# Performance work log

Hardware: AMD Instinct MI355X
Metric: run time of the kernel (lower is better)

Reference implementation:

```python
import jax, jax.numpy as jnp
import numpy as np

W_WORKERS = 2
Q_LEN = 16
HIDDEN = 4096
N_HEADS = 32
N_KV = 8
HEAD_DIM = 128
L_SHARED = 8192
L_WORKER = 2048
THETA = 10000.0


def rotate_half(x):
    x1, x2 = jnp.split(x, 2, axis=-1)
    return jnp.concatenate((-x2, x1), axis=-1)


def rope_cos_sin(pos):
    # pos: int array [...]; returns cos,sin of shape [..., HEAD_DIM] (HF convention: freqs duplicated)
    inv = 1.0 / (THETA ** (jnp.arange(0, HEAD_DIM, 2, dtype=jnp.float32) / HEAD_DIM))
    ang = pos[..., None].astype(jnp.float32) * inv
    emb = jnp.concatenate((ang, ang), axis=-1)
    return jnp.cos(emb), jnp.sin(emb)


def setup_inputs() -> dict:
    key = jax.random.key(0)
    ks = jax.random.split(key, 16)
    std = 0.02
    # new keys are appended at positions L_WORKER..L_WORKER+Q-1 of each worker's own segment
    pos_new = jnp.broadcast_to(L_WORKER + jnp.arange(Q_LEN), (W_WORKERS, Q_LEN))
    cos_new, sin_new = rope_cos_sin(pos_new)
    return {
        'hidden_states': jax.random.normal(ks[0], (W_WORKERS, Q_LEN, HIDDEN), jnp.float32),
        'Wq': jax.random.normal(ks[1], (N_HEADS * HEAD_DIM, HIDDEN), jnp.float32) * std,
        'bq': jnp.zeros((N_HEADS * HEAD_DIM,), jnp.float32),
        'Wk': jax.random.normal(ks[2], (N_KV * HEAD_DIM, HIDDEN), jnp.float32) * std,
        'bk': jnp.zeros((N_KV * HEAD_DIM,), jnp.float32),
        'Wv': jax.random.normal(ks[3], (N_KV * HEAD_DIM, HIDDEN), jnp.float32) * std,
        'bv': jnp.zeros((N_KV * HEAD_DIM,), jnp.float32),
        'Wo': jax.random.normal(ks[4], (HIDDEN, N_HEADS * HEAD_DIM), jnp.float32) * std,
        'seg_shared_k': jax.random.normal(ks[5], (N_KV, L_SHARED, HEAD_DIM), jnp.float32),
        'seg_shared_v': jax.random.normal(ks[6], (N_KV, L_SHARED, HEAD_DIM), jnp.float32),
        'w0_k': jax.random.normal(ks[7], (N_KV, L_WORKER, HEAD_DIM), jnp.float32),
        'w0_v': jax.random.normal(ks[8], (N_KV, L_WORKER, HEAD_DIM), jnp.float32),
        'w1_k': jax.random.normal(ks[9], (N_KV, L_WORKER, HEAD_DIM), jnp.float32),
        'w1_v': jax.random.normal(ks[10], (N_KV, L_WORKER, HEAD_DIM), jnp.float32),
        'cos_new': cos_new,
        'sin_new': sin_new,
    }


def reference(hidden_states, Wq, bq, Wk, bk, Wv, bv, Wo,
              seg_shared_k, seg_shared_v, w0_k, w0_v, w1_k, w1_v,
              cos_new, sin_new):
    W, Q, _ = hidden_states.shape
    scale = HEAD_DIM ** -0.5
    # projections -> [W, n_heads, Q, D]
    q = (hidden_states @ Wq.T + bq).reshape(W, Q, N_HEADS, HEAD_DIM).transpose(0, 2, 1, 3)
    k_new = (hidden_states @ Wk.T + bk).reshape(W, Q, N_KV, HEAD_DIM).transpose(0, 2, 1, 3)
    v_new = (hidden_states @ Wv.T + bv).reshape(W, Q, N_KV, HEAD_DIM).transpose(0, 2, 1, 3)
    # rope new keys (unsqueeze_dim=1: broadcast over kv heads)
    c, s = cos_new[:, None], sin_new[:, None]
    k_new = k_new * c + rotate_half(k_new) * s
    # cache update: segment 0 = shared prompt, segment 1/2 = worker 0/1 own cache (grows by Q)
    keys = [seg_shared_k,
            jnp.concatenate([w0_k, k_new[0]], axis=1),
            jnp.concatenate([w1_k, k_new[1]], axis=1)]
    values = [seg_shared_v,
              jnp.concatenate([w0_v, v_new[0]], axis=1),
              jnp.concatenate([w1_v, v_new[1]], axis=1)]
    frag_lens = [L_SHARED, L_WORKER + Q, L_WORKER + Q]
    # worker w's view: [shared, other worker's cache, own cache]
    orders = [[0, 2, 1], [0, 1, 2]]
    loc = np.zeros((3, W_WORKERS, Q), dtype=np.int32)
    for w, order in enumerate(orders):
        pos = 0
        for seg in reversed(order):
            pos += frag_lens[seg]
            loc[seg, w] = np.arange(pos - Q, pos)
    loc = jnp.asarray(loc)  # [S, W, Q]
    cos_q, sin_q = rope_cos_sin(loc)  # [S, W, Q, D]
    # hogwild_rope: queries rotated per (segment, worker) location -> [S, W, H, Q, D]
    rq = q[None] * cos_q[:, :, None] + rotate_half(q)[None] * sin_q[:, :, None]
    rep = N_HEADS // N_KV
    scores, v_parts = [], []
    for seg in range(3):
        k_s = jnp.repeat(keys[seg], rep, axis=0)  # GQA expand [H, L_s, D]
        sc = jnp.einsum('whqd,hld->whql', rq[seg], k_s) * scale
        mask = jnp.arange(frag_lens[seg])[None, None, None, :] <= loc[seg][:, None, :, None]
        scores.append(jnp.where(mask, sc, jnp.finfo(sc.dtype).min))
        v_parts.append(jnp.repeat(values[seg], rep, axis=0))
    scores = jnp.concatenate(scores, axis=-1)        # [W, H, Q, Ltot] joint softmax over fragments
    probs = jax.nn.softmax(scores, axis=-1)
    v_all = jnp.concatenate(v_parts, axis=1)         # [H, Ltot, D]
    attn = jnp.einsum('whql,hld->whqd', probs, v_all)
    out = attn.transpose(0, 2, 1, 3).reshape(W, Q, N_HEADS * HEAD_DIM) @ Wo.T
    return out
```

## Files before the change

### kernel.cpp

```cpp
#include <hip/hip_runtime.h>
#include <hip/hip_fp16.h>
#include <cstdint>
#include <cstddef>

#define QL 16
#define LSH 8192
#define LWK 2048
#define SCALE 0.08838834764831845f

typedef __attribute__((ext_vector_type(8))) short short8;
typedef __attribute__((ext_vector_type(4))) short short4v;
typedef __attribute__((ext_vector_type(4))) float f32x4;
typedef __attribute__((ext_vector_type(8))) unsigned short ushort8v;

#if defined(__has_builtin)
#if __has_builtin(__builtin_amdgcn_mfma_f32_16x16x16bf16_1k)
#define HAVE_MFMA16 1
#endif
#endif

__device__ __forceinline__ unsigned short f2bf(float f) {
  unsigned int u = __float_as_uint(f);
  u += 0x7fffu + ((u >> 16) & 1u);
  return (unsigned short)(u >> 16);
}
__device__ __forceinline__ float bf2f(unsigned short b) {
  return __uint_as_float(((unsigned int)b) << 16);
}

__device__ __forceinline__ void gload_lds16(const float* g, float* lds) {
  __builtin_amdgcn_global_load_lds(
      (const __attribute__((address_space(1))) void*)g,
      (__attribute__((address_space(3))) void*)lds, 16, 0, 0);
}

__device__ __forceinline__ void gload_f4(float4& d, const float* p) {
  asm volatile("global_load_dwordx4 %0, %1, off"
               : "=v"(d)
               : "v"((const __attribute__((address_space(1))) float*)p));
}
__device__ __forceinline__ void gload_f1(float& d, const float* p) {
  asm volatile("global_load_dword %0, %1, off"
               : "=v"(d)
               : "v"((const __attribute__((address_space(1))) float*)p));
}
__device__ __forceinline__ void gload_s8(short8& d, const unsigned short* p) {
  asm volatile("global_load_dwordx4 %0, %1, off"
               : "=v"(d)
               : "v"((const __attribute__((address_space(1))) unsigned short*)p));
}

__global__ __launch_bounds__(256) void k_cast(
    const float* __restrict__ in, unsigned short* __restrict__ outp, int n4)
{
  int i = blockIdx.x * 256 + threadIdx.x;
  if (i < n4) {
    float4 v = ((const float4*)in)[i];
    ushort4 p; p.x = f2bf(v.x); p.y = f2bf(v.y); p.z = f2bf(v.z); p.w = f2bf(v.w);
    ((ushort4*)outp)[i] = p;
  }
}

__global__ __launch_bounds__(256, 2) void k_gemm4(
    const unsigned short* __restrict__ Xbf,
    const float* __restrict__ W0, const float* __restrict__ W1, const float* __restrict__ W2,
    const float* __restrict__ b0, const float* __restrict__ b1, const float* __restrict__ b2,
    float* __restrict__ outA, float* __restrict__ outB,
    float* __restrict__ outC, float* __restrict__ outD, int Ntot)
{
  __shared__ float Ws[2][16 * 516];
  const int bx = blockIdx.x;
  const int n0 = (bx >> 2) * 16;
  const int kq = bx & 3;
  const float* W; const float* bias; int row0;
  if (n0 < 4096)      { W = W0; bias = b0; row0 = n0; }
  else if (n0 < 5120) { W = W1; bias = b1; row0 = n0 - 4096; }
  else                { W = W2; bias = b2; row0 = n0 - 5120; }
  const int t = threadIdx.x;
  const int w_id = t >> 6;
  const int lane = t & 63;
  const int l15 = lane & 15;
  const int quad = lane >> 4;
  const int cb0 = kq * 1024;
  const int wk = w_id * 128;

  f32x4 C0 = {0.f,0.f,0.f,0.f}, C1 = {0.f,0.f,0.f,0.f};
  short8 xa0[2][4], xa1[2][4];

#pragma unroll
  for (int c = 0; c < 2; ++c) {
    const int cbase = cb0 + c * 512;
#pragma unroll
    for (int i = 0; i < 8; ++i) {
      int idx = w_id * 8 + i;
      int r = idx >> 1, hh = idx & 1;
      const float* g = W + (size_t)(row0 + r) * 4096 + cbase + hh * 256 + lane * 4;
      gload_lds16(g, &Ws[c][r * 516 + hh * 256]);
    }
#pragma unroll
    for (int ks = 0; ks < 4; ++ks) {
      int ko = wk + ks * 32 + quad * 8;
      gload_s8(xa0[c][ks], Xbf + (size_t)l15 * 4096 + cbase + ko);
      gload_s8(xa1[c][ks], Xbf + (size_t)(16 + l15) * 4096 + cbase + ko);
    }
  }
  __builtin_amdgcn_sched_barrier(0);
#pragma unroll
  for (int c = 0; c < 2; ++c) {
    if (c == 0) asm volatile("s_waitcnt vmcnt(16)" ::: "memory");
    else        asm volatile("s_waitcnt vmcnt(0)"  ::: "memory");
    __builtin_amdgcn_sched_barrier(0);
    __builtin_amdgcn_s_barrier();
    __builtin_amdgcn_sched_barrier(0);
    const float* Wsb = Ws[c];
#pragma unroll
    for (int ks = 0; ks < 4; ++ks) {
      int ko = wk + ks * 32 + quad * 8;
      f32x4 wlo = *(const f32x4*)(&Wsb[l15 * 516 + ko]);
      f32x4 whi = *(const f32x4*)(&Wsb[l15 * 516 + ko + 4]);
      short8 bfr;
      bfr[0] = (short)f2bf(wlo[0]); bfr[1] = (short)f2bf(wlo[1]);
      bfr[2] = (short)f2bf(wlo[2]); bfr[3] = (short)f2bf(wlo[3]);
      bfr[4] = (short)f2bf(whi[0]); bfr[5] = (short)f2bf(whi[1]);
      bfr[6] = (short)f2bf(whi[2]); bfr[7] = (short)f2bf(whi[3]);
      C0 = __builtin_amdgcn_mfma_f32_16x16x32_bf16(xa0[c][ks], bfr, C0, 0, 0, 0);
      C1 = __builtin_amdgcn_mfma_f32_16x16x32_bf16(xa1[c][ks], bfr, C1, 0, 0, 0);
    }
  }
  float* Red = &Ws[0][0];
#pragma unroll
  for (int i = 0; i < 4; ++i) {
    Red[w_id * 512 + (quad * 4 + i) * 16 + l15] = C0[i];
    Red[w_id * 512 + 256 + (quad * 4 + i) * 16 + l15] = C1[i];
  }
  __syncthreads();
  float* dst = (kq == 0) ? outA : (kq == 1) ? outB : (kq == 2) ? outC : outD;
#pragma unroll
  for (int e = t; e < 512; e += 256) {
    float s = Red[e] + Red[512 + e] + Red[1024 + e] + Red[1536 + e];
    int m = e >> 4, n = e & 15;
    if (kq == 0 && bias) s += bias[row0 + n];
    dst[(size_t)m * Ntot + n0 + n] = s;
  }
}

__global__ __launch_bounds__(256) void k_add(
    const float* __restrict__ A, const float* __restrict__ B,
    const float* __restrict__ C, const float* __restrict__ D,
    float* __restrict__ o, int n4)
{
  int i = blockIdx.x * 256 + threadIdx.x;
  if (i < n4) {
    float4 a = ((const float4*)A)[i], b = ((const float4*)B)[i];
    float4 c = ((const float4*)C)[i], d = ((const float4*)D)[i];
    float4 r;
    r.x = (a.x + b.x) + (c.x + d.x); r.y = (a.y + b.y) + (c.y + d.y);
    r.z = (a.z + b.z) + (c.z + d.z); r.w = (a.w + b.w) + (c.w + d.w);
    ((float4*)o)[i] = r;
  }
}

__global__ __launch_bounds__(256) void k_rope(
    const float* __restrict__ qA, const float* __restrict__ qB,
    const float* __restrict__ qC, const float* __restrict__ qD,
    const float* __restrict__ cosn, const float* __restrict__ sinn,
    unsigned short* __restrict__ rq, unsigned short* __restrict__ knew,
    unsigned short* __restrict__ vnew)
{
  const int g = blockIdx.x * 256 + threadIdx.x;
  const float LOGTH = 9.210340371976184f;
  if (g < 393216) {
    int d = g & 127, q = (g >> 7) & 15, head = (g >> 11) & 31, w = (g >> 16) & 1, var = g >> 17;
    int tok = w * 16 + q;
    int col = head * 128 + d;
    size_t ix = (size_t)tok * 6144 + col;
    float val = (qA[ix] + qB[ix]) + (qC[ix] + qD[ix]);
    size_t ir = (d < 64) ? ix + 64 : ix - 64;
    float rot = (qA[ir] + qB[ir]) + (qC[ir] + qD[ir]);
    if (d < 64) rot = -rot;
    int pos = (var == 0 ? 12304 : (var == 1 ? 4112 : 2048)) + q;
    int i = d & 63;
    float inv = expf(-(float)i * (LOGTH / 64.0f));
    float ang = (float)pos * inv;
    float c = cosf(ang), s = sinf(ang);
    rq[g] = f2bf((val * c + rot * s) * SCALE);
  } else {
    int g2 = g - 393216;
    if (g2 < 65536) {
      int isv = (g2 >= 32768);
      if (isv) g2 -= 32768;
      int d = g2 & 127, q = (g2 >> 7) & 15, h = (g2 >> 11) & 7, w = (g2 >> 14) & 1;
      int tok = w * 16 + q;
      if (isv) {
        size_t ix = (size_t)tok * 6144 + 5120 + h * 128 + d;
        vnew[g2] = f2bf((qA[ix] + qB[ix]) + (qC[ix] + qD[ix]));
      } else {
        size_t ix = (size_t)tok * 6144 + 4096 + h * 128 + d;
        float val = (qA[ix] + qB[ix]) + (qC[ix] + qD[ix]);
        size_t ir = (d < 64) ? ix + 64 : ix - 64;
        float rot = (qA[ir] + qB[ir]) + (qC[ir] + qD[ir]);
        if (d < 64) rot = -rot;
        float c = cosn[tok * 128 + d], s = sinn[tok * 128 + d];
        knew[g2] = f2bf(val * c + rot * s);
      }
    }
  }
}

__global__ __launch_bounds__(512, 2) void k_attn(
    const float* __restrict__ shk, const float* __restrict__ shv,
    const float* __restrict__ w0k, const float* __restrict__ w0v,
    const float* __restrict__ w1k, const float* __restrict__ w1v,
    const unsigned short* __restrict__ rq,
    const unsigned short* __restrict__ knew, const unsigned short* __restrict__ vnew,
    __half* __restrict__ accP, float* __restrict__ lP)
{
  __shared__ alignas(16) unsigned short Ks[64 * 136];
  __shared__ alignas(16) unsigned short Vts[128 * 72];
#ifndef HAVE_MFMA16
  __shared__ alignas(16) unsigned short Plds[8 * 16 * 72];
#endif

  const int h = blockIdx.x / 98;
  const int cidx = blockIdx.x % 98;
  int kind, k0, nk; bool is_new;
  if (cidx < 64)      { kind = 0; k0 = cidx * 128; nk = 128; is_new = false; }
  else if (cidx < 81) { int c = cidx - 64; kind = 1; k0 = c * 128; nk = (c == 16) ? 16 : 128; is_new = (c == 16); }
  else                { int c = cidx - 81; kind = 2; k0 = c * 128; nk = (c == 16) ? 16 : 128; is_new = (c == 16); }

  const int t = threadIdx.x;
  const int w_id = t >> 6;
  const int lane = t & 63;
  const int l15 = lane & 15;
  const int quad = lane >> 4;
  const int worker = w_id >> 2;
  const int hq = w_id & 3;
  const int col4 = t & 31;
  const int rowb = t >> 5;
  const int dv = t & 127;
  const int tg = t >> 7;

  int var; bool causal;
  if (kind == 0)      { var = 0; causal = false; }
  else if (kind == 1) { var = (worker == 0) ? 2 : 1; causal = (worker == 0); }
  else                { var = (worker == 1) ? 2 : 1; causal = (worker == 1); }

  const float* Ksrc = (kind == 0) ? (shk + (size_t)h * LSH * 128)
                     : (kind == 1) ? (w0k + (size_t)h * LWK * 128)
                                   : (w1k + (size_t)h * LWK * 128);
  const float* Vsrc = (kind == 0) ? (shv + (size_t)h * LSH * 128)
                     : (kind == 1) ? (w0v + (size_t)h * LWK * 128)
                                   : (w1v + (size_t)h * LWK * 128);
  const int wseg = (kind == 2) ? 1 : 0;
  const unsigned short* knsrc = knew + ((size_t)wseg * 8 + h) * 16 * 128;
  const unsigned short* vnsrc = vnew + ((size_t)wseg * 8 + h) * 16 * 128;

  const int head = h * 4 + hq;
  short8 arq[4];
  {
    const unsigned short* base =
        rq + ((((size_t)var * 2 + worker) * 32 + head) * 16 + l15) * 128 + quad * 8;
#pragma unroll
    for (int ks = 0; ks < 4; ++ks) arq[ks] = *(const short8*)(base + ks * 32);
  }

  float lrow = 0.f;
  f32x4 acc[8];
#pragma unroll
  for (int dt = 0; dt < 8; ++dt) acc[dt] = {0.f,0.f,0.f,0.f};

  float4 kf[4];
  float  vf[16];

  const float* kbase = Ksrc + (size_t)(k0 + rowb) * 128 + col4 * 4;
  const float* vbase = Vsrc + (size_t)(k0 + tg * 8) * 128 + dv;

  auto issue_tile = [&](int st) {
    const float* kp = kbase + (size_t)st * 64 * 128;
#pragma unroll
    for (int i = 0; i < 4; ++i) gload_f4(kf[i], kp + (size_t)i * 16 * 128);
    const float* vp = vbase + (size_t)st * 64 * 128;
#pragma unroll
    for (int g = 0; g < 2; ++g)
#pragma unroll
      for (int i = 0; i < 8; ++i)
        gload_f1(vf[g * 8 + i], vp + (size_t)(g * 32 + i) * 128);
  };

  auto lds_write = [&]() {
#pragma unroll
    for (int i = 0; i < 4; ++i) {
      ushort4 p; p.x = f2bf(kf[i].x); p.y = f2bf(kf[i].y);
      p.z = f2bf(kf[i].z); p.w = f2bf(kf[i].w);
      *(ushort4*)(&Ks[(i * 16 + rowb) * 136 + col4 * 4]) = p;
    }
#pragma unroll
    for (int g = 0; g < 2; ++g) {
      ushort8v p;
#pragma unroll
      for (int i = 0; i < 8; ++i) p[i] = f2bf(vf[g * 8 + i]);
      *(ushort8v*)(&Vts[dv * 72 + (g * 4 + tg) * 8]) = p;
    }
  };

  auto compute = [&](int st) {
    f32x4 S[4];
#pragma unroll
    for (int nt = 0; nt < 4; ++nt) S[nt] = {0.f,0.f,0.f,0.f};
#pragma unroll
    for (int ks = 0; ks < 4; ++ks)
#pragma unroll
      for (int nt = 0; nt < 4; ++nt) {
        short8 kfr = *(const short8*)(&Ks[(nt * 16 + l15) * 136 + ks * 32 + quad * 8]);
        S[nt] = __builtin_amdgcn_mfma_f32_16x16x32_bf16(kfr, arq[ks], S[nt], 0, 0, 0);
      }
    if (is_new) {
#pragma unroll
      for (int nt = 0; nt < 4; ++nt)
#pragma unroll
        for (int i = 0; i < 4; ++i) {
          int loc = st * 64 + nt * 16 + quad * 4 + i;
          if (loc >= nk || (causal && loc > l15)) S[nt][i] = -3.0e38f;
        }
    }
    float rs = 0.0f;
#pragma unroll
    for (int nt = 0; nt < 4; ++nt)
#pragma unroll
      for (int i = 0; i < 4; ++i) {
        float p = __expf(fminf(S[nt][i], 60.0f));
        S[nt][i] = p;
        rs += p;
      }
#ifdef HAVE_MFMA16
    short4v pv[4];
#pragma unroll
    for (int nt = 0; nt < 4; ++nt) {
      short4v pp;
      pp[0] = (short)f2bf(S[nt][0]); pp[1] = (short)f2bf(S[nt][1]);
      pp[2] = (short)f2bf(S[nt][2]); pp[3] = (short)f2bf(S[nt][3]);
      pv[nt] = pp;
    }
#else
#pragma unroll
    for (int nt = 0; nt < 4; ++nt)
#pragma unroll
      for (int i = 0; i < 4; ++i)
        Plds[w_id * (16 * 72) + l15 * 72 + nt * 16 + quad * 4 + i] = f2bf(S[nt][i]);
#endif
    rs += __shfl_xor(rs, 16, 64);
    rs += __shfl_xor(rs, 32, 64);
    lrow += rs;

#ifdef HAVE_MFMA16
#pragma unroll
    for (int dt = 0; dt < 8; ++dt)
#pragma unroll
      for (int kc = 0; kc < 4; ++kc) {
        short4v vfr = *(const short4v*)(&Vts[(dt * 16 + l15) * 72 + kc * 16 + quad * 4]);
        acc[dt] = __builtin_amdgcn_mfma_f32_16x16x16bf16_1k(pv[kc], vfr, acc[dt], 0, 0, 0);
      }
#else
    short8 ap[2];
#pragma unroll
    for (int ks2 = 0; ks2 < 2; ++ks2)
      ap[ks2] = *(const short8*)(
          &Plds[w_id * (16 * 72) + l15 * 72 + ks2 * 32 + quad * 8]);
#pragma unroll
    for (int dt = 0; dt < 8; ++dt)
#pragma unroll
      for (int ks2 = 0; ks2 < 2; ++ks2) {
        short8 vfr = *(const short8*)(&Vts[(dt * 16 + l15) * 72 + ks2 * 32 + quad * 8]);
        acc[dt] = __builtin_amdgcn_mfma_f32_16x16x32_bf16(ap[ks2], vfr, acc[dt], 0, 0, 0);
      }
#endif
  };

  const int nst = (nk == 16) ? 1 : 2;
  if (!is_new) {
    issue_tile(0);
  } else {
#pragma unroll
    for (int i = 0; i < 4; ++i) {
      ushort4 p = *(const ushort4*)(knsrc + (size_t)((i * 16 + rowb) & 15) * 128 + col4 * 4);
      kf[i].x = bf2f(p.x); kf[i].y = bf2f(p.y);
      kf[i].z = bf2f(p.z); kf[i].w = bf2f(p.w);
    }
#pragma unroll
    for (int g = 0; g < 2; ++g)
#pragma unroll
      for (int i = 0; i < 8; ++i)
        vf[g * 8 + i] = bf2f(vnsrc[(size_t)((g * 32 + tg * 8 + i) & 15) * 128 + dv]);
  }

  asm volatile("s_waitcnt vmcnt(0)" ::: "memory");
  __builtin_amdgcn_sched_barrier(0);
  lds_write();
  if (nst > 1) issue_tile(1);
  asm volatile("s_waitcnt lgkmcnt(0)" ::: "memory");
  __builtin_amdgcn_sched_barrier(0);
  __builtin_amdgcn_s_barrier();
  __builtin_amdgcn_sched_barrier(0);
  compute(0);

  if (nst > 1) {
    __syncthreads();
    asm volatile("s_waitcnt vmcnt(0)" ::: "memory");
    __builtin_amdgcn_sched_barrier(0);
    lds_write();
    asm volatile("s_waitcnt lgkmcnt(0)" ::: "memory");
    __builtin_amdgcn_sched_barrier(0);
    __builtin_amdgcn_s_barrier();
    __builtin_amdgcn_sched_barrier(0);
    compute(1);
  }

  __half* accB = accP + (size_t)blockIdx.x * 128 * 128;
  const int wrow = worker * 64 + hq * 16;
#pragma unroll
  for (int dt = 0; dt < 8; ++dt)
#pragma unroll
    for (int i = 0; i < 4; ++i) {
      int row = wrow + quad * 4 + i;
      int d = dt * 16 + l15;
      accB[row * 128 + d] = __float2half(acc[dt][i]);
    }
  if (quad == 0) {
    int row = wrow + l15;
    lP[(size_t)blockIdx.x * 128 + row] = lrow;
  }
}

__global__ __launch_bounds__(128) void k_combine(
    const __half* __restrict__ accP, const float* __restrict__ lP,
    unsigned short* __restrict__ attnX)
{
  __shared__ float sl[98];
  const int h = blockIdx.x >> 7;
  const int r = blockIdx.x & 127;
  const int d = threadIdx.x;
  if (d < 98) sl[d] = lP[(size_t)(h * 98 + d) * 128 + r];
  __syncthreads();
  float L = 0.0f, A = 0.0f;
#pragma unroll
  for (int c = 0; c < 98; ++c) L += sl[c];
#pragma unroll
  for (int cc = 0; cc < 98; cc += 7) {
    float p[7];
#pragma unroll
    for (int i = 0; i < 7; ++i)
      p[i] = __half2float(accP[((size_t)(h * 98 + cc + i) * 128 + r) * 128 + d]);
#pragma unroll
    for (int i = 0; i < 7; ++i) A += p[i];
  }
  int workerv = r >> 6, hqv = (r >> 4) & 3, q = r & 15;
  int head = h * 4 + hqv;
  attnX[(size_t)(workerv * 16 + q) * 4096 + head * 128 + d] = f2bf(A / L);
}

extern "C" void kernel_launch(void* const* d_in, const int* in_sizes, int n_in,
                              void* d_out, int out_size, void* d_ws, size_t ws_size,
                              hipStream_t stream)
{
  const float* hs   = (const float*)d_in[0];
  const float* Wq   = (const float*)d_in[1];
  const float* bq   = (const float*)d_in[2];
  const float* Wk   = (const float*)d_in[3];
  const float* bk   = (const float*)d_in[4];
  const float* Wv   = (const float*)d_in[5];
  const float* bv   = (const float*)d_in[6];
  const float* Wo   = (const float*)d_in[7];
  const float* shk  = (const float*)d_in[8];
  const float* shv  = (const float*)d_in[9];
  const float* w0k  = (const float*)d_in[10];
  const float* w0v  = (const float*)d_in[11];
  const float* w1k  = (const float*)d_in[12];
  const float* w1v  = (const float*)d_in[13];
  const float* cosn = (const float*)d_in[14];
  const float* sinn = (const float*)d_in[15];
  float* out = (float*)d_out;

  char* ws = (char*)d_ws;
  unsigned short* rq     = (unsigned short*)(ws + 0);
  unsigned short* knew   = (unsigned short*)(ws + 786432);
  unsigned short* vnew   = (unsigned short*)(ws + 851968);
  unsigned short* hsbf   = (unsigned short*)(ws + 917504);
  unsigned short* attnXb = (unsigned short*)(ws + 1179648);
  float*          lP     = (float*)(ws + 1441792);
  __half*         accP   = (__half*)(ws + 1843200);
  float*          qkvA   = (float*)(ws + 1843200);
  float*          qkvB   = (float*)(ws + 1843200 + 786432);
  float*          qkvC   = (float*)(ws + 1843200 + 2 * 786432);
  float*          qkvD   = (float*)(ws + 1843200 + 3 * 786432);
  float*          outA   = (float*)(ws + 1843200);
  float*          outB   = (float*)(ws + 1843200 + 524288);
  float*          outC   = (float*)(ws + 1843200 + 2 * 524288);
  float*          outD   = (float*)(ws + 1843200 + 3 * 524288);

  k_cast<<<128, 256, 0, stream>>>(hs, hsbf, 32768);
  k_gemm4<<<1536, 256, 0, stream>>>(hsbf, Wq, Wk, Wv, bq, bk, bv,
                                    qkvA, qkvB, qkvC, qkvD, 6144);
  k_rope<<<1792, 256, 0, stream>>>(qkvA, qkvB, qkvC, qkvD, cosn, sinn, rq, knew, vnew);
  k_attn<<<784, 512, 0, stream>>>(shk, shv, w0k, w0v, w1k, w1v, rq, knew, vnew, accP, lP);
  k_combine<<<1024, 128, 0, stream>>>(accP, lP, attnXb);
  k_gemm4<<<1024, 256, 0, stream>>>(attnXb, Wo, Wo, Wo, nullptr, nullptr, nullptr,
                                    outA, outB, outC, outD, 4096);
  k_add<<<128, 256, 0, stream>>>(outA, outB, outC, outD, out, 32768);
}
```

Before: 296.1 us.

## Fuse input cast into GEMM, load weights directly, prefetch both attention tiles

The separate fp32-to-bf16 cast kernel is removed. The GEMM now reads fp32 hidden states and converts them in registers, and it loads weight rows straight from global memory instead of staging them in LDS. It runs with an occupancy hint of 8 blocks. The attention kernel issues global loads for both K/V tiles up front into separate register sets and waits partially, so the second tile's fetch overlaps the first tile's compute, with an occupancy hint of 4. This removes a kernel launch and LDS staging, but raises register pressure and leaves the global weight loads uncoalesced across lanes, with each lane reading a different row.

```diff
diff --git a/kernel.cpp b/kernel.cpp
--- a/kernel.cpp
+++ b/kernel.cpp
@@ -28,12 +28,6 @@
   return __uint_as_float(((unsigned int)b) << 16);
 }
 
-__device__ __forceinline__ void gload_lds16(const float* g, float* lds) {
-  __builtin_amdgcn_global_load_lds(
-      (const __attribute__((address_space(1))) void*)g,
-      (__attribute__((address_space(3))) void*)lds, 16, 0, 0);
-}
-
 __device__ __forceinline__ void gload_f4(float4& d, const float* p) {
   asm volatile("global_load_dwordx4 %0, %1, off"
                : "=v"(d)
@@ -44,31 +38,15 @@
                : "=v"(d)
                : "v"((const __attribute__((address_space(1))) float*)p));
 }
-__device__ __forceinline__ void gload_s8(short8& d, const unsigned short* p) {
-  asm volatile("global_load_dwordx4 %0, %1, off"
-               : "=v"(d)
-               : "v"((const __attribute__((address_space(1))) unsigned short*)p));
-}
-
-__global__ __launch_bounds__(256) void k_cast(
-    const float* __restrict__ in, unsigned short* __restrict__ outp, int n4)
-{
-  int i = blockIdx.x * 256 + threadIdx.x;
-  if (i < n4) {
-    float4 v = ((const float4*)in)[i];
-    ushort4 p; p.x = f2bf(v.x); p.y = f2bf(v.y); p.z = f2bf(v.z); p.w = f2bf(v.w);
-    ((ushort4*)outp)[i] = p;
-  }
-}
-
-__global__ __launch_bounds__(256, 2) void k_gemm4(
-    const unsigned short* __restrict__ Xbf,
+
+__global__ __launch_bounds__(256, 8) void k_gemm(
+    const float* __restrict__ Xf, const unsigned short* __restrict__ Xb,
     const float* __restrict__ W0, const float* __restrict__ W1, const float* __restrict__ W2,
     const float* __restrict__ b0, const float* __restrict__ b1, const float* __restrict__ b2,
     float* __restrict__ outA, float* __restrict__ outB,
-    float* __restrict__ outC, float* __restrict__ outD, int Ntot)
-{
-  __shared__ float Ws[2][16 * 516];
+    float* __restrict__ outC, float* __restrict__ outD, int Ntot, int xf32)
+{
+  __shared__ float Red[2048];
   const int bx = blockIdx.x;
   const int n0 = (bx >> 2) * 16;
   const int kq = bx & 3;
@@ -81,53 +59,43 @@
   const int lane = t & 63;
   const int l15 = lane & 15;
   const int quad = lane >> 4;
-  const int cb0 = kq * 1024;
-  const int wk = w_id * 128;
+  const int wk = kq * 1024 + w_id * 256;
 
   f32x4 C0 = {0.f,0.f,0.f,0.f}, C1 = {0.f,0.f,0.f,0.f};
-  short8 xa0[2][4], xa1[2][4];
-
-#pragma unroll
-  for (int c = 0; c < 2; ++c) {
-    const int cbase = cb0 + c * 512;
-#pragma unroll
-    for (int i = 0; i < 8; ++i) {
-      int idx = w_id * 8 + i;
-      int r = idx >> 1, hh = idx & 1;
-      const float* g = W + (size_t)(row0 + r) * 4096 + cbase + hh * 256 + lane * 4;
-      gload_lds16(g, &Ws[c][r * 516 + hh * 256]);
-    }
-#pragma unroll
-    for (int ks = 0; ks < 4; ++ks) {
-      int ko = wk + ks * 32 + quad * 8;
-      gload_s8(xa0[c][ks], Xbf + (size_t)l15 * 4096 + cbase + ko);
-      gload_s8(xa1[c][ks], Xbf + (size_t)(16 + l15) * 4096 + cbase + ko);
-    }
-  }
-  __builtin_amdgcn_sched_barrier(0);
-#pragma unroll
-  for (int c = 0; c < 2; ++c) {
-    if (c == 0) asm volatile("s_waitcnt vmcnt(16)" ::: "memory");
-    else        asm volatile("s_waitcnt vmcnt(0)"  ::: "memory");
-    __builtin_amdgcn_sched_barrier(0);
-    __builtin_amdgcn_s_barrier();
-    __builtin_amdgcn_sched_barrier(0);
-    const float* Wsb = Ws[c];
-#pragma unroll
-    for (int ks = 0; ks < 4; ++ks) {
-      int ko = wk + ks * 32 + quad * 8;
-      f32x4 wlo = *(const f32x4*)(&Wsb[l15 * 516 + ko]);
-      f32x4 whi = *(const f32x4*)(&Wsb[l15 * 516 + ko + 4]);
-      short8 bfr;
-      bfr[0] = (short)f2bf(wlo[0]); bfr[1] = (short)f2bf(wlo[1]);
-      bfr[2] = (short)f2bf(wlo[2]); bfr[3] = (short)f2bf(wlo[3]);
-      bfr[4] = (short)f2bf(whi[0]); bfr[5] = (short)f2bf(whi[1]);
-      bfr[6] = (short)f2bf(whi[2]); bfr[7] = (short)f2bf(whi[3]);
-      C0 = __builtin_amdgcn_mfma_f32_16x16x32_bf16(xa0[c][ks], bfr, C0, 0, 0, 0);
-      C1 = __builtin_amdgcn_mfma_f32_16x16x32_bf16(xa1[c][ks], bfr, C1, 0, 0, 0);
-    }
-  }
-  float* Red = &Ws[0][0];
+  const float* Wr = W + (size_t)(row0 + l15) * 4096;
+
+#pragma unroll
+  for (int ks = 0; ks < 8; ++ks) {
+    const int ko = wk + ks * 32 + quad * 8;
+    f32x4 wlo = *(const f32x4*)(Wr + ko);
+    f32x4 whi = *(const f32x4*)(Wr + ko + 4);
+    short8 bfr;
+    bfr[0] = (short)f2bf(wlo[0]); bfr[1] = (short)f2bf(wlo[1]);
+    bfr[2] = (short)f2bf(wlo[2]); bfr[3] = (short)f2bf(wlo[3]);
+    bfr[4] = (short)f2bf(whi[0]); bfr[5] = (short)f2bf(whi[1]);
+    bfr[6] = (short)f2bf(whi[2]); bfr[7] = (short)f2bf(whi[3]);
+    short8 a0, a1;
+    if (xf32) {
+      f32x4 x0l = *(const f32x4*)(Xf + (size_t)l15 * 4096 + ko);
+      f32x4 x0h = *(const f32x4*)(Xf + (size_t)l15 * 4096 + ko + 4);
+      f32x4 x1l = *(const f32x4*)(Xf + (size_t)(16 + l15) * 4096 + ko);
+      f32x4 x1h = *(const f32x4*)(Xf + (size_t)(16 + l15) * 4096 + ko + 4);
+      a0[0] = (short)f2bf(x0l[0]); a0[1] = (short)f2bf(x0l[1]);
+      a0[2] = (short)f2bf(x0l[2]); a0[3] = (short)f2bf(x0l[3]);
+      a0[4] = (short)f2bf(x0h[0]); a0[5] = (short)f2bf(x0h[1]);
+      a0[6] = (short)f2bf(x0h[2]); a0[7] = (short)f2bf(x0h[3]);
+      a1[0] = (short)f2bf(x1l[0]); a1[1] = (short)f2bf(x1l[1]);
+      a1[2] = (short)f2bf(x1l[2]); a1[3] = (short)f2bf(x1l[3]);
+      a1[4] = (short)f2bf(x1h[0]); a1[5] = (short)f2bf(x1h[1]);
+      a1[6] = (short)f2bf(x1h[2]); a1[7] = (short)f2bf(x1h[3]);
+    } else {
+      a0 = *(const short8*)(Xb + (size_t)l15 * 4096 + ko);
+      a1 = *(const short8*)(Xb + (size_t)(16 + l15) * 4096 + ko);
+    }
+    C0 = __builtin_amdgcn_mfma_f32_16x16x32_bf16(a0, bfr, C0, 0, 0, 0);
+    C1 = __builtin_amdgcn_mfma_f32_16x16x32_bf16(a1, bfr, C1, 0, 0, 0);
+  }
+
 #pragma unroll
   for (int i = 0; i < 4; ++i) {
     Red[w_id * 512 + (quad * 4 + i) * 16 + l15] = C0[i];
@@ -207,7 +175,7 @@
   }
 }
 
-__global__ __launch_bounds__(512, 2) void k_attn(
+__global__ __launch_bounds__(512, 4) void k_attn(
     const float* __restrict__ shk, const float* __restrict__ shv,
     const float* __restrict__ w0k, const float* __restrict__ w0v,
     const float* __restrict__ w1k, const float* __restrict__ w1v,
@@ -269,25 +237,44 @@
 #pragma unroll
   for (int dt = 0; dt < 8; ++dt) acc[dt] = {0.f,0.f,0.f,0.f};
 
-  float4 kf[4];
-  float  vf[16];
+  float4 kf[4], kf2[4];
+  float  vf[16], vf2[16];
 
   const float* kbase = Ksrc + (size_t)(k0 + rowb) * 128 + col4 * 4;
   const float* vbase = Vsrc + (size_t)(k0 + tg * 8) * 128 + dv;
 
-  auto issue_tile = [&](int st) {
-    const float* kp = kbase + (size_t)st * 64 * 128;
-#pragma unroll
-    for (int i = 0; i < 4; ++i) gload_f4(kf[i], kp + (size_t)i * 16 * 128);
-    const float* vp = vbase + (size_t)st * 64 * 128;
+  const int nst = (nk == 16) ? 1 : 2;
+  if (!is_new) {
+#pragma unroll
+    for (int i = 0; i < 4; ++i) gload_f4(kf[i], kbase + (size_t)i * 16 * 128);
 #pragma unroll
     for (int g = 0; g < 2; ++g)
 #pragma unroll
       for (int i = 0; i < 8; ++i)
-        gload_f1(vf[g * 8 + i], vp + (size_t)(g * 32 + i) * 128);
-  };
-
-  auto lds_write = [&]() {
+        gload_f1(vf[g * 8 + i], vbase + (size_t)(g * 32 + i) * 128);
+#pragma unroll
+    for (int i = 0; i < 4; ++i)
+      gload_f4(kf2[i], kbase + (size_t)(64 + i * 16) * 128);
+#pragma unroll
+    for (int g = 0; g < 2; ++g)
+#pragma unroll
+      for (int i = 0; i < 8; ++i)
+        gload_f1(vf2[g * 8 + i], vbase + (size_t)(64 + g * 32 + i) * 128);
+  } else {
+#pragma unroll
+    for (int i = 0; i < 4; ++i) {
+      ushort4 p = *(const ushort4*)(knsrc + (size_t)((i * 16 + rowb) & 15) * 128 + col4 * 4);
+      kf[i].x = bf2f(p.x); kf[i].y = bf2f(p.y);
+      kf[i].z = bf2f(p.z); kf[i].w = bf2f(p.w);
+    }
+#pragma unroll
+    for (int g = 0; g < 2; ++g)
+#pragma unroll
+      for (int i = 0; i < 8; ++i)
+        vf[g * 8 + i] = bf2f(vnsrc[(size_t)((g * 32 + tg * 8 + i) & 15) * 128 + dv]);
+  }
+
+  auto lds_write0 = [&]() {
 #pragma unroll
     for (int i = 0; i < 4; ++i) {
       ushort4 p; p.x = f2bf(kf[i].x); p.y = f2bf(kf[i].y);
@@ -299,6 +286,21 @@
       ushort8v p;
 #pragma unroll
       for (int i = 0; i < 8; ++i) p[i] = f2bf(vf[g * 8 + i]);
+      *(ushort8v*)(&Vts[dv * 72 + (g * 4 + tg) * 8]) = p;
+    }
+  };
+  auto lds_write1 = [&]() {
+#pragma unroll
+    for (int i = 0; i < 4; ++i) {
+      ushort4 p; p.x = f2bf(kf2[i].x); p.y = f2bf(kf2[i].y);
+      p.z = f2bf(kf2[i].z); p.w = f2bf(kf2[i].w);
+      *(ushort4*)(&Ks[(i * 16 + rowb) * 136 + col4 * 4]) = p;
+    }
+#pragma unroll
+    for (int g = 0; g < 2; ++g) {
+      ushort8v p;
+#pragma unroll
+      for (int i = 0; i < 8; ++i) p[i] = f2bf(vf2[g * 8 + i]);
       *(ushort8v*)(&Vts[dv * 72 + (g * 4 + tg) * 8]) = p;
     }
   };
@@ -376,27 +378,10 @@
 #endif
   };
 
-  const int nst = (nk == 16) ? 1 : 2;
-  if (!is_new) {
-    issue_tile(0);
-  } else {
-#pragma unroll
-    for (int i = 0; i < 4; ++i) {
-      ushort4 p = *(const ushort4*)(knsrc + (size_t)((i * 16 + rowb) & 15) * 128 + col4 * 4);
-      kf[i].x = bf2f(p.x); kf[i].y = bf2f(p.y);
-      kf[i].z = bf2f(p.z); kf[i].w = bf2f(p.w);
-    }
-#pragma unroll
-    for (int g = 0; g < 2; ++g)
-#pragma unroll
-      for (int i = 0; i < 8; ++i)
-        vf[g * 8 + i] = bf2f(vnsrc[(size_t)((g * 32 + tg * 8 + i) & 15) * 128 + dv]);
-  }
-
-  asm volatile("s_waitcnt vmcnt(0)" ::: "memory");
+  if (nst > 1) asm volatile("s_waitcnt vmcnt(20)" ::: "memory");
+  else         asm volatile("s_waitcnt vmcnt(0)"  ::: "memory");
   __builtin_amdgcn_sched_barrier(0);
-  lds_write();
-  if (nst > 1) issue_tile(1);
+  lds_write0();
   asm volatile("s_waitcnt lgkmcnt(0)" ::: "memory");
   __builtin_amdgcn_sched_barrier(0);
   __builtin_amdgcn_s_barrier();
@@ -404,10 +389,11 @@
   compute(0);
 
   if (nst > 1) {
-    __syncthreads();
+    __builtin_amdgcn_s_barrier();
+    __builtin_amdgcn_sched_barrier(0);
     asm volatile("s_waitcnt vmcnt(0)" ::: "memory");
     __builtin_amdgcn_sched_barrier(0);
-    lds_write();
+    lds_write1();
     asm volatile("s_waitcnt lgkmcnt(0)" ::: "memory");
     __builtin_amdgcn_sched_barrier(0);
     __builtin_amdgcn_s_barrier();
@@ -484,7 +470,6 @@
   unsigned short* rq     = (unsigned short*)(ws + 0);
   unsigned short* knew   = (unsigned short*)(ws + 786432);
   unsigned short* vnew   = (unsigned short*)(ws + 851968);
-  unsigned short* hsbf   = (unsigned short*)(ws + 917504);
   unsigned short* attnXb = (unsigned short*)(ws + 1179648);
   float*          lP     = (float*)(ws + 1441792);
   __half*         accP   = (__half*)(ws + 1843200);
@@ -497,13 +482,13 @@
   float*          outC   = (float*)(ws + 1843200 + 2 * 524288);
   float*          outD   = (float*)(ws + 1843200 + 3 * 524288);
 
-  k_cast<<<128, 256, 0, stream>>>(hs, hsbf, 32768);
-  k_gemm4<<<1536, 256, 0, stream>>>(hsbf, Wq, Wk, Wv, bq, bk, bv,
-                                    qkvA, qkvB, qkvC, qkvD, 6144);
+  k_gemm<<<1536, 256, 0, stream>>>(hs, nullptr, Wq, Wk, Wv, bq, bk, bv,
+                                   qkvA, qkvB, qkvC, qkvD, 6144, 1);
   k_rope<<<1792, 256, 0, stream>>>(qkvA, qkvB, qkvC, qkvD, cosn, sinn, rq, knew, vnew);
   k_attn<<<784, 512, 0, stream>>>(shk, shv, w0k, w0v, w1k, w1v, rq, knew, vnew, accP, lP);
   k_combine<<<1024, 128, 0, stream>>>(accP, lP, attnXb);
-  k_gemm4<<<1024, 256, 0, stream>>>(attnXb, Wo, Wo, Wo, nullptr, nullptr, nullptr,
-                                    outA, outB, outC, outD, 4096);
+  k_gemm<<<1024, 256, 0, stream>>>(nullptr, attnXb, Wo, Wo, Wo,
+                                   nullptr, nullptr, nullptr,
+                                   outA, outB, outC, outD, 4096, 0);
   k_add<<<128, 256, 0, stream>>>(outA, outB, outC, outD, out, 32768);
 }
```

New measurement: 298.9 us. About the same (+0.9%).
